# Kernel optimization log

Measured on AMD Instinct MI355X. Metric: run time of the kernel, lower is better.

## Reference

```python
import jax, jax.numpy as jnp
import numpy as np

N_SIN = 3  # fcn_n_sin

def _feats(x):
    # x: [B, Din] -> features [B, Din, 1 + 2*N_SIN]
    omega = (2.0 ** jnp.arange(N_SIN, dtype=x.dtype))  # [n_sin]
    ox = x[..., None] * omega  # [B, Din, n_sin]
    return jnp.concatenate([x[..., None], jnp.sin(ox), jnp.cos(ox)], axis=-1)

def setup_inputs() -> dict:
    key = jax.random.key(0)
    k1, k2, k3 = jax.random.split(key, 3)
    B, Din, Dout, H, F = 2048, 64, 64, 32, 1 + 2 * N_SIN
    x = jax.random.normal(k1, (B, Din), dtype=jnp.float32)
    # xavier-normal-ish init for W1/W2, zeros for biases (matches init_parameters)
    W1 = jax.random.normal(k2, (Din, Dout, H, F), dtype=jnp.float32) * np.sqrt(2.0 / (H + F))
    W2 = jax.random.normal(k3, (Din, Dout, 1, H), dtype=jnp.float32) * np.sqrt(2.0 / (1 + H))
    B1 = jnp.zeros((Din, Dout, H), dtype=jnp.float32)
    B2 = jnp.zeros((Din, Dout, 1), dtype=jnp.float32)
    return {"x": x, "W1": W1, "W2": W2, "B1": B1, "B2": B2}

def reference(x, W1, W2, B1, B2):
    f = _feats(x)  # [B, Din, F]
    # per-edge first layer: [B, Din, Dout, H]
    h = jnp.einsum('bif,iohf->bioh', f, W1) + B1[None]
    h = jax.nn.silu(h)
    # per-edge second layer -> scalar: [B, Din, Dout]
    phis = jnp.einsum('bioh,ioh->bio', h, W2[:, :, 0, :]) + B2[:, :, 0][None]
    return phis.sum(axis=1)  # [B, Dout]
```

## Files before the change

### kernel.cpp

```cpp
#include <hip/hip_runtime.h>
#include <math.h>

typedef _Float16 f16;
typedef f16   f16x4    __attribute__((ext_vector_type(4)));
typedef f16   f16x8    __attribute__((ext_vector_type(8)));
typedef float floatx2  __attribute__((ext_vector_type(2)));
typedef float floatx4  __attribute__((ext_vector_type(4)));
typedef float floatx16 __attribute__((ext_vector_type(16)));

#define LOG2E   1.44269504088896340736f
#define INV_2PI 0.15915494309189533577f

#define B_SZ  2048
#define DIN   64
#define DOUT  64
#define NH    32

#define NIG   2
#define IGW   (DIN / NIG)

#define W1IMG_ELEMS ((size_t)DIN * DOUT * 64 * 4)
#define FIMG_ELEMS  ((size_t)DIN * 64 * 64 * 4)
#define W2Q_ELEMS   ((size_t)DIN * DOUT * NH)

__device__ __forceinline__ floatx2 pk_add(floatx2 a, floatx2 b) {
    floatx2 d; asm("v_pk_add_f32 %0, %1, %2" : "=v"(d) : "v"(a), "v"(b)); return d;
}
__device__ __forceinline__ floatx2 pk_mul(floatx2 a, floatx2 b) {
    floatx2 d; asm("v_pk_mul_f32 %0, %1, %2" : "=v"(d) : "v"(a), "v"(b)); return d;
}
__device__ __forceinline__ floatx2 pk_fma(floatx2 a, floatx2 b, floatx2 c) {
    floatx2 d; asm("v_pk_fma_f32 %0, %1, %2, %3" : "=v"(d) : "v"(a), "v"(b), "v"(c)); return d;
}

__global__ __launch_bounds__(256) void prep_kernel(
        const float* __restrict__ W1, const float* __restrict__ B1,
        const float* __restrict__ W2, const float* __restrict__ B2,
        const float* __restrict__ x,
        f16* __restrict__ w1img, f16* __restrict__ fimg,
        float* __restrict__ w2q, float* __restrict__ b2sum,
        float* __restrict__ out) {
    const int bid = blockIdx.x, tid = threadIdx.x;
    if (bid < 512) {
        int u = bid * 256 + tid;
        int lane2 = u & 31, o = (u >> 5) & 63, i = u >> 11;
        int l0 = lane2 * 2;
        f16x8 v;
        if (lane2 < 16) {
#pragma unroll
            for (int t = 0; t < 2; ++t) {
                const float* w = W1 + (size_t)((i * 64 + o) * 32 + l0 + t) * 7;
#pragma unroll
                for (int j = 0; j < 4; ++j) v[t * 4 + j] = (f16)(w[j] * (-LOG2E));
            }
        } else {
#pragma unroll
            for (int t = 0; t < 2; ++t) {
                int m = l0 - 32 + t;
                const float* w = W1 + (size_t)((i * 64 + o) * 32 + m) * 7;
                v[t * 4 + 0] = (f16)(w[4] * (-LOG2E));
                v[t * 4 + 1] = (f16)(w[5] * (-LOG2E));
                v[t * 4 + 2] = (f16)(w[6] * (-LOG2E));
                v[t * 4 + 3] = (f16)(B1[(i * 64 + o) * 32 + m] * (-LOG2E));
            }
        }
        *(f16x8*)(w1img + (size_t)u * 8) = v;
    } else if (bid < 1024) {
        int u = (bid - 512) * 256 + tid;
        int lane2 = u & 31, btp = (u >> 5) & 63, i = u >> 11;
        int l0 = lane2 * 2;
        f16x8 v;
#pragma unroll
        for (int t = 0; t < 2; ++t) {
            int b = btp * 32 + ((l0 + t) & 31);
            float xv = x[b * 64 + i];
            float s1 = __builtin_amdgcn_sinf(xv * INV_2PI);
            float c1 = __builtin_amdgcn_cosf(xv * INV_2PI);
            float s2 = 2.0f * s1 * c1, c2 = 1.0f - 2.0f * s1 * s1;
            float s4 = 2.0f * s2 * c2, c4 = 1.0f - 2.0f * s2 * s2;
            if (lane2 < 16) { v[t*4+0] = (f16)xv; v[t*4+1] = (f16)s1;
                              v[t*4+2] = (f16)s2; v[t*4+3] = (f16)s4; }
            else            { v[t*4+0] = (f16)c1; v[t*4+1] = (f16)c2;
                              v[t*4+2] = (f16)c4; v[t*4+3] = (f16)1.0f; }
        }
        *(f16x8*)(fimg + (size_t)u * 8) = v;
    } else if (bid < 1152) {
        int t = (bid - 1024) * 256 + tid;
        floatx4 v = *(const floatx4*)(W2 + (size_t)t * 4);
        v *= (-1.0f / LOG2E);
        *(floatx4*)(w2q + (size_t)t * 4) = v;
    } else if (bid < 1280) {
        int t = (bid - 1152) * 256 + tid;
        floatx4 z = {};
        *(floatx4*)(out + (size_t)t * 4) = z;
    } else if (tid < 64) {
        float s = 0.0f;
        for (int i = 0; i < 64; ++i) s += B2[i * 64 + tid];
        b2sum[tid] = s;
    }
}

__device__ __forceinline__ void silu8(
        floatx2 A0, floatx2 A1, floatx2 A2, floatx2 A3,
        floatx2 W0, floatx2 W1, floatx2 W2, floatx2 W3,
        floatx2 one2, float& phi) {
    floatx2 E0 = {__builtin_amdgcn_exp2f(A0[0]), __builtin_amdgcn_exp2f(A0[1])};
    floatx2 E1 = {__builtin_amdgcn_exp2f(A1[0]), __builtin_amdgcn_exp2f(A1[1])};
    floatx2 E2 = {__builtin_amdgcn_exp2f(A2[0]), __builtin_amdgcn_exp2f(A2[1])};
    floatx2 E3 = {__builtin_amdgcn_exp2f(A3[0]), __builtin_amdgcn_exp2f(A3[1])};
    floatx2 D0 = pk_add(E0, one2), D1 = pk_add(E1, one2);
    floatx2 D2 = pk_add(E2, one2), D3 = pk_add(E3, one2);
    floatx2 U0 = pk_mul(A0, W0), U1 = pk_mul(A1, W1);
    floatx2 U2 = pk_mul(A2, W2), U3 = pk_mul(A3, W3);
    floatx2 N01 = pk_fma(U0, D1, pk_mul(U1, D0));
    floatx2 N23 = pk_fma(U2, D3, pk_mul(U3, D2));
    floatx2 P01 = pk_mul(D0, D1), P23 = pk_mul(D2, D3);
    floatx2 N   = pk_fma(N01, P23, pk_mul(N23, P01));
    floatx2 DD  = pk_mul(P01, P23);
    float n8 = __builtin_fmaf(N[0], DD[1], N[1] * DD[0]);
    float d8 = DD[0] * DD[1];
    phi = __builtin_fmaf(n8, __builtin_amdgcn_rcpf(d8), phi);
}

__global__ __launch_bounds__(256, 8) void main_kernel(
        const f16* __restrict__ w1img, const f16* __restrict__ fimg,
        const float* __restrict__ w2q, const float* __restrict__ b2sum,
        float* __restrict__ out) {
    const int tid  = threadIdx.x;
    const int lane = tid & 63;
    const int wv   = tid >> 6;
    const int btp  = blockIdx.x & 63;
    const int og   = (blockIdx.x >> 6) & 15;
    const int ig   = blockIdx.x >> 10;
    const int o    = __builtin_amdgcn_readfirstlane(og * 4 + wv);
    const int p    = lane >> 5;
    const size_t ibase = (size_t)ig * IGW;

    __shared__ float ws2[4][IGW][32];
#pragma unroll
    for (int s = 0; s < 4; ++s) {
        int idx = s * 1024 + tid * 4;
        int ii_ = (idx >> 5) & 31, h_ = idx & 31;
        const float* src = w2q + (ibase + ii_) * 2048
                         + (size_t)(og * 4 + s) * 32 + h_;
        *(floatx4*)&ws2[s][ii_][h_] = *(const floatx4*)src;
    }
    __syncthreads();

    const f16* ap = w1img + ibase * 16384 + ((size_t)o   * 64 + lane) * 4;
    const f16* bp = fimg  + ibase * 16384 + ((size_t)btp * 64 + lane) * 4;

    const floatx16 zeroC = {};
    const floatx2  one2  = {1.0f, 1.0f};
    float phiL = 0.0f, phiH = 0.0f;

    f16x4 a0v = *(const f16x4*)ap;
    f16x4 b0v = *(const f16x4*)bp;
    f16x4 a_n = *(const f16x4*)(ap + 16384);
    f16x4 b_n = *(const f16x4*)(bp + 16384);
    floatx16 Ccur = __builtin_amdgcn_mfma_f32_32x32x8f16(a0v, b0v, zeroC, 0, 0, 0);

#pragma unroll 1
    for (int ii = 0; ii < IGW; ++ii) {
        floatx16 Cn = __builtin_amdgcn_mfma_f32_32x32x8f16(a_n, b_n, zeroC, 0, 0, 0);
        const size_t i2 = (size_t)(ii + 2);
        a_n = *(const f16x4*)(ap + i2 * 16384);
        b_n = *(const f16x4*)(bp + i2 * 16384);

        const float* wrow = &ws2[wv][ii][p * 4];
        const floatx4 W0 = *(const floatx4*)(wrow);
        const floatx4 W1v = *(const floatx4*)(wrow + 8);
        const floatx4 W2v = *(const floatx4*)(wrow + 16);
        const floatx4 W3v = *(const floatx4*)(wrow + 24);

        silu8((floatx2){Ccur[0],  Ccur[1]},  (floatx2){Ccur[4],  Ccur[5]},
              (floatx2){Ccur[8],  Ccur[9]},  (floatx2){Ccur[12], Ccur[13]},
              (floatx2){W0[0], W0[1]}, (floatx2){W1v[0], W1v[1]},
              (floatx2){W2v[0], W2v[1]}, (floatx2){W3v[0], W3v[1]},
              one2, phiL);
        silu8((floatx2){Ccur[2],  Ccur[3]},  (floatx2){Ccur[6],  Ccur[7]},
              (floatx2){Ccur[10], Ccur[11]}, (floatx2){Ccur[14], Ccur[15]},
              (floatx2){W0[2], W0[3]}, (floatx2){W1v[2], W1v[3]},
              (floatx2){W2v[2], W2v[3]}, (floatx2){W3v[2], W3v[3]},
              one2, phiH);

        Ccur = Cn;
    }

    float phi = phiL + phiH;
    phi += __shfl_xor(phi, 32, 64);

    if (lane < 32) {
        float v = phi + (1.0f / NIG) * b2sum[o];
        unsafeAtomicAdd(out + (size_t)(btp * 32 + lane) * 64 + o, v);
    }
}

extern "C" void kernel_launch(void* const* d_in, const int* in_sizes, int n_in,
                              void* d_out, int out_size, void* d_ws, size_t ws_size,
                              hipStream_t stream) {
    const float* x  = (const float*)d_in[0];
    const float* W1 = (const float*)d_in[1];
    const float* W2 = (const float*)d_in[2];
    const float* B1 = (const float*)d_in[3];
    const float* B2 = (const float*)d_in[4];
    float* out = (float*)d_out;

    f16*   w1img = (f16*)d_ws;
    f16*   fimg  = w1img + W1IMG_ELEMS;
    float* w2q   = (float*)(fimg + FIMG_ELEMS);
    float* b2sum = w2q + W2Q_ELEMS;

    prep_kernel<<<1281, 256, 0, stream>>>(W1, B1, W2, B2, x, w1img, fimg, w2q, b2sum, out);
    main_kernel<<<NIG * 16 * 64, 256, 0, stream>>>(w1img, fimg, w2q, b2sum, out);
}
```

Baseline: 114.2 us.

## Fuse prep and main kernels into one kernel computing features in LDS

Removes the separate prep kernel and its f16 workspace images. The fused kernel computes the sin/cos features for its batch tile into shared memory, reads and packs W1/B1 from global fp32 on the fly, and reads W2 directly from global with a one-step register prefetch. The input-dimension split and atomics go away, so each block loops over all 64 inputs and writes the output with a plain store. The costs are half the blocks in the grid, a lower occupancy hint, redundant in-loop W1 repacking across blocks, and a per-lane serial B2 sum at the end.

```diff
diff --git a/kernel.cpp b/kernel.cpp
--- a/kernel.cpp
+++ b/kernel.cpp
@@ -3,7 +3,6 @@
 
 typedef _Float16 f16;
 typedef f16   f16x4    __attribute__((ext_vector_type(4)));
-typedef f16   f16x8    __attribute__((ext_vector_type(8)));
 typedef float floatx2  __attribute__((ext_vector_type(2)));
 typedef float floatx4  __attribute__((ext_vector_type(4)));
 typedef float floatx16 __attribute__((ext_vector_type(16)));
@@ -16,13 +15,6 @@
 #define DOUT  64
 #define NH    32
 
-#define NIG   2
-#define IGW   (DIN / NIG)
-
-#define W1IMG_ELEMS ((size_t)DIN * DOUT * 64 * 4)
-#define FIMG_ELEMS  ((size_t)DIN * 64 * 64 * 4)
-#define W2Q_ELEMS   ((size_t)DIN * DOUT * NH)
-
 __device__ __forceinline__ floatx2 pk_add(floatx2 a, floatx2 b) {
     floatx2 d; asm("v_pk_add_f32 %0, %1, %2" : "=v"(d) : "v"(a), "v"(b)); return d;
 }
@@ -33,71 +25,16 @@
     floatx2 d; asm("v_pk_fma_f32 %0, %1, %2, %3" : "=v"(d) : "v"(a), "v"(b), "v"(c)); return d;
 }
 
-__global__ __launch_bounds__(256) void prep_kernel(
-        const float* __restrict__ W1, const float* __restrict__ B1,
-        const float* __restrict__ W2, const float* __restrict__ B2,
-        const float* __restrict__ x,
-        f16* __restrict__ w1img, f16* __restrict__ fimg,
-        float* __restrict__ w2q, float* __restrict__ b2sum,
-        float* __restrict__ out) {
-    const int bid = blockIdx.x, tid = threadIdx.x;
-    if (bid < 512) {
-        int u = bid * 256 + tid;
-        int lane2 = u & 31, o = (u >> 5) & 63, i = u >> 11;
-        int l0 = lane2 * 2;
-        f16x8 v;
-        if (lane2 < 16) {
-#pragma unroll
-            for (int t = 0; t < 2; ++t) {
-                const float* w = W1 + (size_t)((i * 64 + o) * 32 + l0 + t) * 7;
-#pragma unroll
-                for (int j = 0; j < 4; ++j) v[t * 4 + j] = (f16)(w[j] * (-LOG2E));
-            }
-        } else {
-#pragma unroll
-            for (int t = 0; t < 2; ++t) {
-                int m = l0 - 32 + t;
-                const float* w = W1 + (size_t)((i * 64 + o) * 32 + m) * 7;
-                v[t * 4 + 0] = (f16)(w[4] * (-LOG2E));
-                v[t * 4 + 1] = (f16)(w[5] * (-LOG2E));
-                v[t * 4 + 2] = (f16)(w[6] * (-LOG2E));
-                v[t * 4 + 3] = (f16)(B1[(i * 64 + o) * 32 + m] * (-LOG2E));
-            }
-        }
-        *(f16x8*)(w1img + (size_t)u * 8) = v;
-    } else if (bid < 1024) {
-        int u = (bid - 512) * 256 + tid;
-        int lane2 = u & 31, btp = (u >> 5) & 63, i = u >> 11;
-        int l0 = lane2 * 2;
-        f16x8 v;
-#pragma unroll
-        for (int t = 0; t < 2; ++t) {
-            int b = btp * 32 + ((l0 + t) & 31);
-            float xv = x[b * 64 + i];
-            float s1 = __builtin_amdgcn_sinf(xv * INV_2PI);
-            float c1 = __builtin_amdgcn_cosf(xv * INV_2PI);
-            float s2 = 2.0f * s1 * c1, c2 = 1.0f - 2.0f * s1 * s1;
-            float s4 = 2.0f * s2 * c2, c4 = 1.0f - 2.0f * s2 * s2;
-            if (lane2 < 16) { v[t*4+0] = (f16)xv; v[t*4+1] = (f16)s1;
-                              v[t*4+2] = (f16)s2; v[t*4+3] = (f16)s4; }
-            else            { v[t*4+0] = (f16)c1; v[t*4+1] = (f16)c2;
-                              v[t*4+2] = (f16)c4; v[t*4+3] = (f16)1.0f; }
-        }
-        *(f16x8*)(fimg + (size_t)u * 8) = v;
-    } else if (bid < 1152) {
-        int t = (bid - 1024) * 256 + tid;
-        floatx4 v = *(const floatx4*)(W2 + (size_t)t * 4);
-        v *= (-1.0f / LOG2E);
-        *(floatx4*)(w2q + (size_t)t * 4) = v;
-    } else if (bid < 1280) {
-        int t = (bid - 1152) * 256 + tid;
-        floatx4 z = {};
-        *(floatx4*)(out + (size_t)t * 4) = z;
-    } else if (tid < 64) {
-        float s = 0.0f;
-        for (int i = 0; i < 64; ++i) s += B2[i * 64 + tid];
-        b2sum[tid] = s;
-    }
+__device__ __forceinline__ floatx4 load4u(const float* p) {
+    floatx4 v; __builtin_memcpy(&v, p, 16); return v;
+}
+
+__device__ __forceinline__ f16x4 packA(floatx4 w, float b1v, bool hi) {
+    float g0 = (hi ? w[1] : w[0]) * (-LOG2E);
+    float g1 = (hi ? w[2] : w[1]) * (-LOG2E);
+    float g2 = (hi ? w[3] : w[2]) * (-LOG2E);
+    float g3 = (hi ? b1v  : w[3]) * (-LOG2E);
+    return (f16x4){(f16)g0, (f16)g1, (f16)g2, (f16)g3};
 }
 
 __device__ __forceinline__ void silu8(
@@ -122,77 +59,104 @@
     phi = __builtin_fmaf(n8, __builtin_amdgcn_rcpf(d8), phi);
 }
 
-__global__ __launch_bounds__(256, 8) void main_kernel(
-        const f16* __restrict__ w1img, const f16* __restrict__ fimg,
-        const float* __restrict__ w2q, const float* __restrict__ b2sum,
-        float* __restrict__ out) {
+__global__ __launch_bounds__(256, 4) void fused_kernel(
+        const float* __restrict__ x,  const float* __restrict__ W1,
+        const float* __restrict__ B1, const float* __restrict__ W2,
+        const float* __restrict__ B2, float* __restrict__ out) {
     const int tid  = threadIdx.x;
     const int lane = tid & 63;
     const int wv   = tid >> 6;
     const int btp  = blockIdx.x & 63;
-    const int og   = (blockIdx.x >> 6) & 15;
-    const int ig   = blockIdx.x >> 10;
+    const int og   = blockIdx.x >> 6;
     const int o    = __builtin_amdgcn_readfirstlane(og * 4 + wv);
-    const int p    = lane >> 5;
-    const size_t ibase = (size_t)ig * IGW;
+    const int h    = lane & 31;
+    const bool hi  = lane >= 32;
 
-    __shared__ float ws2[4][IGW][32];
+    __shared__ f16 flds[64][256];
+
+    {
+        int bl = tid >> 3, i0 = (tid & 7) * 8;
+        const float* xp = x + ((size_t)(btp * 32 + bl)) * 64 + i0;
+        floatx4 xa = *(const floatx4*)xp;
+        floatx4 xb = *(const floatx4*)(xp + 4);
 #pragma unroll
-    for (int s = 0; s < 4; ++s) {
-        int idx = s * 1024 + tid * 4;
-        int ii_ = (idx >> 5) & 31, h_ = idx & 31;
-        const float* src = w2q + (ibase + ii_) * 2048
-                         + (size_t)(og * 4 + s) * 32 + h_;
-        *(floatx4*)&ws2[s][ii_][h_] = *(const floatx4*)src;
+        for (int k = 0; k < 8; ++k) {
+            float xv = k < 4 ? xa[k & 3] : xb[k & 3];
+            float xr = xv * INV_2PI;
+            float s1 = __builtin_amdgcn_sinf(xr);
+            float c1 = __builtin_amdgcn_cosf(xr);
+            float s2 = 2.0f * s1 * c1, c2 = 1.0f - 2.0f * s1 * s1;
+            float s4 = 2.0f * s2 * c2, c4 = 1.0f - 2.0f * s2 * s2;
+            f16x4 vlo = {(f16)xv, (f16)s1, (f16)s2, (f16)s4};
+            f16x4 vhi = {(f16)c1, (f16)c2, (f16)c4, (f16)1.0f};
+            int i = i0 + k;
+            *(f16x4*)&flds[i][bl * 4]        = vlo;
+            *(f16x4*)&flds[i][(bl + 32) * 4] = vhi;
+        }
     }
     __syncthreads();
 
-    const f16* ap = w1img + ibase * 16384 + ((size_t)o   * 64 + lane) * 4;
-    const f16* bp = fimg  + ibase * 16384 + ((size_t)btp * 64 + lane) * 4;
+    const float* w1p = W1 + (size_t)(o * 32 + h) * 7 + (hi ? 3 : 0);
+    const float* b1p = B1 + o * 32 + h;
+    const float* w2p = W2 + (size_t)o * 32 + (hi ? 4 : 0);
 
     const floatx16 zeroC = {};
     const floatx2  one2  = {1.0f, 1.0f};
     float phiL = 0.0f, phiH = 0.0f;
 
-    f16x4 a0v = *(const f16x4*)ap;
-    f16x4 b0v = *(const f16x4*)bp;
-    f16x4 a_n = *(const f16x4*)(ap + 16384);
-    f16x4 b_n = *(const f16x4*)(bp + 16384);
-    floatx16 Ccur = __builtin_amdgcn_mfma_f32_32x32x8f16(a0v, b0v, zeroC, 0, 0, 0);
+    floatx4 rw  = load4u(w1p);
+    float   rb  = *b1p;
+    f16x4   rbf = *(const f16x4*)&flds[0][lane * 4];
+    floatx4 w2c0 = *(const floatx4*)(w2p);
+    floatx4 w2c1 = *(const floatx4*)(w2p + 8);
+    floatx4 w2c2 = *(const floatx4*)(w2p + 16);
+    floatx4 w2c3 = *(const floatx4*)(w2p + 24);
+    floatx16 C0 = __builtin_amdgcn_mfma_f32_32x32x8f16(packA(rw, rb, hi), rbf, zeroC, 0, 0, 0);
+    rw  = load4u(w1p + 14336);
+    rb  = b1p[2048];
+    rbf = *(const f16x4*)&flds[1][lane * 4];
+    floatx4 w2n0 = *(const floatx4*)(w2p + 2048);
+    floatx4 w2n1 = *(const floatx4*)(w2p + 2048 + 8);
+    floatx4 w2n2 = *(const floatx4*)(w2p + 2048 + 16);
+    floatx4 w2n3 = *(const floatx4*)(w2p + 2048 + 24);
 
 #pragma unroll 1
-    for (int ii = 0; ii < IGW; ++ii) {
-        floatx16 Cn = __builtin_amdgcn_mfma_f32_32x32x8f16(a_n, b_n, zeroC, 0, 0, 0);
-        const size_t i2 = (size_t)(ii + 2);
-        a_n = *(const f16x4*)(ap + i2 * 16384);
-        b_n = *(const f16x4*)(bp + i2 * 16384);
+    for (int ii = 0; ii < 64; ++ii) {
+        floatx16 C1 = __builtin_amdgcn_mfma_f32_32x32x8f16(packA(rw, rb, hi), rbf, zeroC, 0, 0, 0);
 
-        const float* wrow = &ws2[wv][ii][p * 4];
-        const floatx4 W0 = *(const floatx4*)(wrow);
-        const floatx4 W1v = *(const floatx4*)(wrow + 8);
-        const floatx4 W2v = *(const floatx4*)(wrow + 16);
-        const floatx4 W3v = *(const floatx4*)(wrow + 24);
+        const size_t inx = (size_t)(ii + 2 <= 63 ? ii + 2 : 63);
+        rw  = load4u(w1p + inx * 14336);
+        rb  = b1p[inx * 2048];
+        rbf = *(const f16x4*)&flds[inx][lane * 4];
 
-        silu8((floatx2){Ccur[0],  Ccur[1]},  (floatx2){Ccur[4],  Ccur[5]},
-              (floatx2){Ccur[8],  Ccur[9]},  (floatx2){Ccur[12], Ccur[13]},
-              (floatx2){W0[0], W0[1]}, (floatx2){W1v[0], W1v[1]},
-              (floatx2){W2v[0], W2v[1]}, (floatx2){W3v[0], W3v[1]},
+        silu8((floatx2){C0[0],  C0[1]},  (floatx2){C0[4],  C0[5]},
+              (floatx2){C0[8],  C0[9]},  (floatx2){C0[12], C0[13]},
+              (floatx2){w2c0[0], w2c0[1]}, (floatx2){w2c1[0], w2c1[1]},
+              (floatx2){w2c2[0], w2c2[1]}, (floatx2){w2c3[0], w2c3[1]},
               one2, phiL);
-        silu8((floatx2){Ccur[2],  Ccur[3]},  (floatx2){Ccur[6],  Ccur[7]},
-              (floatx2){Ccur[10], Ccur[11]}, (floatx2){Ccur[14], Ccur[15]},
-              (floatx2){W0[2], W0[3]}, (floatx2){W1v[2], W1v[3]},
-              (floatx2){W2v[2], W2v[3]}, (floatx2){W3v[2], W3v[3]},
+        silu8((floatx2){C0[2],  C0[3]},  (floatx2){C0[6],  C0[7]},
+              (floatx2){C0[10], C0[11]}, (floatx2){C0[14], C0[15]},
+              (floatx2){w2c0[2], w2c0[3]}, (floatx2){w2c1[2], w2c1[3]},
+              (floatx2){w2c2[2], w2c2[3]}, (floatx2){w2c3[2], w2c3[3]},
               one2, phiH);
 
-        Ccur = Cn;
+        w2c0 = w2n0; w2c1 = w2n1; w2c2 = w2n2; w2c3 = w2n3;
+        w2n0 = *(const floatx4*)(w2p + inx * 2048);
+        w2n1 = *(const floatx4*)(w2p + inx * 2048 + 8);
+        w2n2 = *(const floatx4*)(w2p + inx * 2048 + 16);
+        w2n3 = *(const floatx4*)(w2p + inx * 2048 + 24);
+
+        C0 = C1;
     }
 
     float phi = phiL + phiH;
     phi += __shfl_xor(phi, 32, 64);
 
     if (lane < 32) {
-        float v = phi + (1.0f / NIG) * b2sum[o];
-        unsafeAtomicAdd(out + (size_t)(btp * 32 + lane) * 64 + o, v);
+        float b2s = 0.0f;
+#pragma unroll 1
+        for (int i2 = 0; i2 < 64; ++i2) b2s += B2[i2 * 64 + o];
+        out[((size_t)btp * 32 + lane) * 64 + o] = phi * (-1.0f / LOG2E) + b2s;
     }
 }
 
@@ -205,12 +169,7 @@
     const float* B1 = (const float*)d_in[3];
     const float* B2 = (const float*)d_in[4];
     float* out = (float*)d_out;
+    (void)d_ws; (void)ws_size;
 
-    f16*   w1img = (f16*)d_ws;
-    f16*   fimg  = w1img + W1IMG_ELEMS;
-    float* w2q   = (float*)(fimg + FIMG_ELEMS);
-    float* b2sum = w2q + W2Q_ELEMS;
-
-    prep_kernel<<<1281, 256, 0, stream>>>(W1, B1, W2, B2, x, w1img, fimg, w2q, b2sum, out);
-    main_kernel<<<NIG * 16 * 64, 256, 0, stream>>>(w1img, fimg, w2q, b2sum, out);
+    fused_kernel<<<16 * 64, 256, 0, stream>>>(x, W1, B1, W2, B2, out);
 }
```

New measurement: 140.3 us. +22.8%, slower.
